# Performance work log

Hardware: AMD Instinct MI355X
Metric: run time of the kernel (lower is better)

The kernel has to match this reference:

```python
import jax, jax.numpy as jnp
import numpy as np

K_RATIO = 0.01
SIM_THRESHOLD = 0.6


def _gcn_update(feats, W_gcn, b_gcn):
    # feats: [N, C]. Build edges: inverse_similarity < (1 - thr)/2  <=>  cos sim > thr.
    nf = feats / jnp.maximum(jnp.linalg.norm(feats, axis=1, keepdims=True), 1e-12)
    sim = nf @ nf.T                                  # [N, N]
    inv_sim = (1.0 - sim) * 0.5
    adj = (inv_sim < (1.0 - SIM_THRESHOLD) * 0.5).astype(feats.dtype)  # includes self loops
    deg = jnp.sum(adj, axis=1)
    dinv = jax.lax.rsqrt(jnp.maximum(deg, 1.0))      # D^{-1/2}
    agg = dinv[:, None] * (adj @ (dinv[:, None] * feats))
    return agg @ W_gcn + b_gcn                        # [N, C]


def setup_inputs() -> dict:
    key = jax.random.key(0)
    k1, k2, k3 = jax.random.split(key, 3)
    B, C, H, W = 16, 128, 160, 160
    z = jax.random.normal(k1, (B, C, H, W), dtype=jnp.float32)
    score = jax.random.uniform(k2, (B, H, W), dtype=jnp.float32)
    W_gcn = jax.random.normal(k3, (C, C), dtype=jnp.float32) * (1.0 / np.sqrt(C))
    b_gcn = jnp.zeros((C,), dtype=jnp.float32)
    return {"z": z, "score": score, "W_gcn": W_gcn, "b_gcn": b_gcn}


def reference(z, score, W_gcn, b_gcn):
    B, C, H, W = z.shape
    num_select = int(H * W * K_RATIO)                # 256, static
    flat_score = score.reshape(B, H * W)
    _, top_idx = jax.lax.top_k(flat_score, num_select)   # [B, S]

    flat_z = z.reshape(B, C, H * W)
    idx_bcs = jnp.broadcast_to(top_idx[:, None, :], (B, C, num_select))
    top_features = jnp.take_along_axis(flat_z, idx_bcs, axis=2)  # [B, C, S]
    feats = top_features.transpose(0, 2, 1).reshape(B * num_select, C)  # [N, C]

    updated = _gcn_update(feats, W_gcn, b_gcn)        # [N, C]
    updated = updated.reshape(B, num_select, C).transpose(0, 2, 1)  # [B, C, S]

    b_ix = jnp.arange(B)[:, None, None]
    c_ix = jnp.arange(C)[None, :, None]
    new_flat = flat_z.at[b_ix, c_ix, top_idx[:, None, :]].set(updated)
    return new_flat.reshape(B, C, H, W)
```

## Files before the change

kernel.cpp:

```cpp
#include <hip/hip_runtime.h>
#include <hip/hip_bf16.h>

#define HWs 25600
#define NB 16
#define NC 128
#define NS 256
#define NN 4096
#define N4 13107200

#define K1_CPB 2880
#define K2_CPB 2240
#define K3_CPB 1280
#define CP_U 8
#define K2_BASE 5898240
#define K3_BASE 10485760

typedef __attribute__((ext_vector_type(8))) short bf16x8;
typedef __attribute__((ext_vector_type(4))) float f32x4;
typedef __attribute__((ext_vector_type(4))) int i32x4;
typedef unsigned long long u64;

template <int U>
__device__ __forceinline__ void copy_slice(const float4* __restrict__ zz,
                                           float4* __restrict__ oo,
                                           size_t base, int cb, int tid) {
  size_t start = base + (size_t)cb * (U * 256) + tid;
  float4 v[U];
  #pragma unroll
  for (int k = 0; k < U; ++k) v[k] = zz[start + k * 256];
  __builtin_amdgcn_sched_barrier(0);
  #pragma unroll
  for (int k = 0; k < U; ++k) oo[start + k * 256] = v[k];
}

__global__ __launch_bounds__(256) void k1_kernel(const float* __restrict__ z,
                                                 const float* __restrict__ score,
                                                 float* __restrict__ out,
                                                 int* __restrict__ sel) {
  __shared__ int hist[256];
  __shared__ int scan_s[256];
  __shared__ int scan_eq[256];
  __shared__ int bc_dig, bc_k;
  const int tid = threadIdx.x;
  const int bid = blockIdx.x;

  if (bid >= NB) {
    copy_slice<CP_U>((const float4*)z, (float4*)out, 0, bid - NB, tid);
    return;
  }

  int b = bid;
  const float* sc = score + (size_t)b * HWs;
  const float4* sc4 = (const float4*)sc;

  unsigned prefix = 0; int k = NS;
  for (int d = 3; d >= 0; --d) {
    int sh = d * 8;
    hist[tid] = 0; __syncthreads();
    unsigned maskHigh = (d == 3) ? 0u : (0xFFFFFFFFu << (sh + 8));
    #pragma unroll 5
    for (int i4 = 0; i4 < 25; ++i4) {
      float4 f = sc4[tid * 25 + i4];
      const float* fp = (const float*)&f;
      #pragma unroll
      for (int c = 0; c < 4; ++c) {
        unsigned v = __float_as_uint(fp[c]);
        if ((v & maskHigh) == prefix) atomicAdd(&hist[(v >> sh) & 255], 1);
      }
    }
    __syncthreads();
    int val = hist[255 - tid];
    scan_s[tid] = val; __syncthreads();
    for (int off = 1; off < 256; off <<= 1) {
      int a = (tid >= off) ? scan_s[tid - off] : 0;
      __syncthreads();
      scan_s[tid] += a; __syncthreads();
    }
    int q = 255 - tid;
    int Sq = scan_s[tid];
    int before = Sq - hist[q];
    if (before < k && k <= Sq) { bc_dig = q; bc_k = k - before; }
    __syncthreads();
    prefix |= ((unsigned)bc_dig) << sh;
    k = bc_k;
    __syncthreads();
  }
  unsigned t = prefix;

  int cgt = 0, ceq = 0;
  #pragma unroll 5
  for (int i4 = 0; i4 < 25; ++i4) {
    float4 f = sc4[tid * 25 + i4];
    const float* fp = (const float*)&f;
    #pragma unroll
    for (int c = 0; c < 4; ++c) {
      unsigned v = __float_as_uint(fp[c]);
      cgt += (v > t) ? 1 : 0;
      ceq += (v == t) ? 1 : 0;
    }
  }
  scan_s[tid] = cgt; scan_eq[tid] = ceq; __syncthreads();
  for (int off = 1; off < 256; off <<= 1) {
    int ag = (tid >= off) ? scan_s[tid - off] : 0;
    int ae = (tid >= off) ? scan_eq[tid - off] : 0;
    __syncthreads();
    scan_s[tid] += ag; scan_eq[tid] += ae; __syncthreads();
  }
  int total_gt = scan_s[255];
  int need = NS - total_gt;
  int g = scan_s[tid] - cgt;
  int e = scan_eq[tid] - ceq;
  for (int i4 = 0; i4 < 25; ++i4) {
    float4 f = sc4[tid * 25 + i4];
    const float* fp = (const float*)&f;
    #pragma unroll
    for (int c = 0; c < 4; ++c) {
      int i = tid * 100 + i4 * 4 + c;
      unsigned v = __float_as_uint(fp[c]);
      if (v > t) { sel[b * NS + g] = i; ++g; }
      else if (v == t) { if (e < need) sel[b * NS + total_gt + e] = i; ++e; }
    }
  }
}

__global__ __launch_bounds__(256) void k2_kernel(const float* __restrict__ z,
                                                 const int* __restrict__ sel,
                                                 float* __restrict__ out,
                                                 float* __restrict__ feats,
                                                 ushort* __restrict__ nfb) {
  const int tid = threadIdx.x;
  const int bid = blockIdx.x;
  if (bid >= NN / 4) {
    copy_slice<CP_U>((const float4*)z, (float4*)out, K2_BASE, bid - NN / 4, tid);
    return;
  }
  int row = bid * 4 + (tid >> 6);
  int lane = tid & 63;
  int b = row >> 8;
  int idx = sel[row];
  const float* zb = z + (size_t)b * NC * HWs + idx;
  float v0 = zb[(size_t)lane * HWs];
  float v1 = zb[(size_t)(lane + 64) * HWs];
  float ss = v0 * v0 + v1 * v1;
  #pragma unroll
  for (int off = 32; off; off >>= 1) ss += __shfl_xor(ss, off);
  float denom = fmaxf(sqrtf(ss), 1e-12f);
  feats[row * NC + lane] = v0;
  feats[row * NC + lane + 64] = v1;
  __hip_bfloat16 h0 = __float2bfloat16(v0 / denom);
  __hip_bfloat16 h1 = __float2bfloat16(v1 / denom);
  nfb[row * NC + lane] = *reinterpret_cast<ushort*>(&h0);
  nfb[row * NC + lane + 64] = *reinterpret_cast<ushort*>(&h1);
}

__global__ __launch_bounds__(256) void k3_kernel(const ushort* __restrict__ nfb,
                                                 const float* __restrict__ z,
                                                 float* __restrict__ out,
                                                 u64* __restrict__ adj) {
  __shared__ __align__(16) ushort tA[64 * 128];
  __shared__ __align__(16) ushort tB[64 * 128];
  __shared__ u64 rowbits[64];
  const int tid = threadIdx.x;
  const int bid = blockIdx.x;
  if (bid >= 4096) {
    copy_slice<CP_U>((const float4*)z, (float4*)out, K3_BASE, bid - 4096, tid);
    return;
  }
  int I0 = (bid & 63) * 64, J0 = (bid >> 6) * 64;
  if (tid < 64) rowbits[tid] = 0ull;
  for (int f = tid; f < 1024; f += 256) {
    int r = f >> 4, c = f & 15;
    int scnk = c ^ (r & 7);
    *(i32x4*)&tA[r * 128 + scnk * 8] = *(const i32x4*)(nfb + (size_t)(I0 + r) * NC + c * 8);
    *(i32x4*)&tB[r * 128 + scnk * 8] = *(const i32x4*)(nfb + (size_t)(J0 + r) * NC + c * 8);
  }
  __syncthreads();
  int w = tid >> 6, l = tid & 63;
  int r = l & 15, kg = l >> 4;
  f32x4 acc[4] = {{0.f, 0.f, 0.f, 0.f}, {0.f, 0.f, 0.f, 0.f},
                  {0.f, 0.f, 0.f, 0.f}, {0.f, 0.f, 0.f, 0.f}};
  int Ar = 16 * w + r;
  #pragma unroll
  for (int kk = 0; kk < 4; ++kk) {
    int chunkA = (kk * 4 + kg) ^ (Ar & 7);
    bf16x8 a = *(bf16x8*)&tA[Ar * 128 + chunkA * 8];
    #pragma unroll
    for (int j = 0; j < 4; ++j) {
      int Bc = 16 * j + r;
      int chunkB = (kk * 4 + kg) ^ (Bc & 7);
      bf16x8 bf = *(bf16x8*)&tB[Bc * 128 + chunkB * 8];
      acc[j] = __builtin_amdgcn_mfma_f32_16x16x32_bf16(a, bf, acc[j], 0, 0, 0);
    }
  }
  #pragma unroll
  for (int q = 0; q < 4; ++q) {
    u64 m = 0ull;
    #pragma unroll
    for (int j = 0; j < 4; ++j) {
      float simv = acc[j][q];
      if ((1.0f - simv) * 0.5f < 0.2f) m |= 1ull << (16 * j + (l & 15));
    }
    if (m) atomicOr(&rowbits[16 * w + (l >> 4) * 4 + q], m);
  }
  __syncthreads();
  if (tid < 64) adj[(size_t)(I0 + tid) * 64 + (bid >> 6)] = rowbits[tid];
}

__global__ __launch_bounds__(256) void k4_kernel(const u64* __restrict__ adj,
                                                 const float* __restrict__ feats,
                                                 const float* __restrict__ Wg,
                                                 const float* __restrict__ bg,
                                                 const int* __restrict__ sel,
                                                 float* __restrict__ out) {
  __shared__ __align__(16) float Wt[NC * 132];
  __shared__ __align__(16) float aggT[16 * 132];
  int tid = threadIdx.x;
  int r0 = blockIdx.x * 16;
  for (int f = tid; f < NC * NC; f += 256) {
    int c = f >> 7, cp = f & 127;
    Wt[cp * 132 + c] = Wg[f];
  }
  int w = tid >> 6, lane = tid & 63;
  for (int rr = 0; rr < 4; ++rr) {
    int lrow = w * 4 + rr;
    int row = r0 + lrow;
    u64 mw = adj[(size_t)row * 64 + lane];
    int ctot = __popcll(mw);
    #pragma unroll
    for (int off = 32; off; off >>= 1) ctot += __shfl_xor(ctot, off);
    float dinv_i = 1.0f / sqrtf(fmaxf((float)ctot, 1.0f));
    float acc0 = 0.f, acc1 = 0.f;
    for (int wi = 0; wi < 64; ++wi) {
      u64 w64 = __shfl((long long)mw, wi);
      while (w64) {
        int bit = __builtin_ctzll(w64);
        w64 &= w64 - 1;
        int j = wi * 64 + bit;
        u64 jm = adj[(size_t)j * 64 + lane];
        int cj = __popcll(jm);
        #pragma unroll
        for (int off = 32; off; off >>= 1) cj += __shfl_xor(cj, off);
        float dj = 1.0f / sqrtf(fmaxf((float)cj, 1.0f));
        acc0 += dj * feats[(size_t)j * NC + lane];
        acc1 += dj * feats[(size_t)j * NC + lane + 64];
      }
    }
    aggT[lrow * 132 + lane] = dinv_i * acc0;
    aggT[lrow * 132 + lane + 64] = dinv_i * acc1;
  }
  __syncthreads();
  int cp = tid & 127;
  int rsub = tid >> 7;
  float acc[8];
  float bb = bg[cp];
  #pragma unroll
  for (int q = 0; q < 8; ++q) acc[q] = bb;
  for (int c4 = 0; c4 < 32; ++c4) {
    float4 w4 = *(const float4*)&Wt[cp * 132 + c4 * 4];
    #pragma unroll
    for (int q = 0; q < 8; ++q) {
      float4 a4 = *(const float4*)&aggT[(rsub + 2 * q) * 132 + c4 * 4];
      acc[q] += a4.x * w4.x + a4.y * w4.y + a4.z * w4.z + a4.w * w4.w;
    }
  }
  #pragma unroll
  for (int q = 0; q < 8; ++q) {
    int row = r0 + rsub + 2 * q;
    int batch = row >> 8;
    int idx = sel[row];
    out[(size_t)(batch * NC + cp) * HWs + idx] = acc[q];
  }
}

extern "C" void kernel_launch(void* const* d_in, const int* in_sizes, int n_in,
                              void* d_out, int out_size, void* d_ws, size_t ws_size,
                              hipStream_t stream) {
  const float* z     = (const float*)d_in[0];
  const float* score = (const float*)d_in[1];
  const float* Wg    = (const float*)d_in[2];
  const float* bg    = (const float*)d_in[3];
  float* out = (float*)d_out;

  char* ws = (char*)d_ws;
  size_t off = 0;
  auto alloc = [&](size_t bytes) {
    void* p = ws + off;
    off = (off + bytes + 255) & ~(size_t)255;
    return p;
  };
  int* sel     = (int*)alloc(NN * sizeof(int));
  float* feats = (float*)alloc((size_t)NN * NC * sizeof(float));
  ushort* nfb  = (ushort*)alloc((size_t)NN * NC * sizeof(ushort));
  u64* adj     = (u64*)alloc((size_t)NN * 64 * sizeof(u64));

  k1_kernel<<<NB + K1_CPB, 256, 0, stream>>>(z, score, out, sel);
  k2_kernel<<<NN / 4 + K2_CPB, 256, 0, stream>>>(z, sel, out, feats, nfb);
  k3_kernel<<<4096 + K3_CPB, 256, 0, stream>>>(nfb, z, out, adj);
  k4_kernel<<<256, 256, 0, stream>>>(adj, feats, Wg, bg, sel, out);
}
```

Baseline: 178.1 us.

## Move full z copy into k1, use nontemporal stores, precompute degrees via atomics

```diff
diff --git a/kernel.cpp b/kernel.cpp
--- a/kernel.cpp
+++ b/kernel.cpp
@@ -7,13 +7,8 @@
 #define NS 256
 #define NN 4096
 #define N4 13107200
-
-#define K1_CPB 2880
-#define K2_CPB 2240
-#define K3_CPB 1280
 #define CP_U 8
-#define K2_BASE 5898240
-#define K3_BASE 10485760
+#define K1_CPB 6400
 
 typedef __attribute__((ext_vector_type(8))) short bf16x8;
 typedef __attribute__((ext_vector_type(4))) float f32x4;
@@ -23,14 +18,15 @@
 template <int U>
 __device__ __forceinline__ void copy_slice(const float4* __restrict__ zz,
                                            float4* __restrict__ oo,
-                                           size_t base, int cb, int tid) {
-  size_t start = base + (size_t)cb * (U * 256) + tid;
+                                           int cb, int tid) {
+  size_t start = (size_t)cb * (U * 256) + tid;
   float4 v[U];
   #pragma unroll
   for (int k = 0; k < U; ++k) v[k] = zz[start + k * 256];
   __builtin_amdgcn_sched_barrier(0);
   #pragma unroll
-  for (int k = 0; k < U; ++k) oo[start + k * 256] = v[k];
+  for (int k = 0; k < U; ++k)
+    __builtin_nontemporal_store(*(const f32x4*)&v[k], (f32x4*)&oo[start + k * 256]);
 }
 
 __global__ __launch_bounds__(256) void k1_kernel(const float* __restrict__ z,
@@ -45,7 +41,7 @@
   const int bid = blockIdx.x;
 
   if (bid >= NB) {
-    copy_slice<CP_U>((const float4*)z, (float4*)out, 0, bid - NB, tid);
+    copy_slice<CP_U>((const float4*)z, (float4*)out, bid - NB, tid);
     return;
   }
 
@@ -125,14 +121,13 @@
 
 __global__ __launch_bounds__(256) void k2_kernel(const float* __restrict__ z,
                                                  const int* __restrict__ sel,
-                                                 float* __restrict__ out,
                                                  float* __restrict__ feats,
-                                                 ushort* __restrict__ nfb) {
+                                                 ushort* __restrict__ nfb,
+                                                 int* __restrict__ deg) {
   const int tid = threadIdx.x;
   const int bid = blockIdx.x;
-  if (bid >= NN / 4) {
-    copy_slice<CP_U>((const float4*)z, (float4*)out, K2_BASE, bid - NN / 4, tid);
-    return;
+  if (bid < 4) {
+    *(i32x4*)&deg[bid * 1024 + tid * 4] = (i32x4){0, 0, 0, 0};
   }
   int row = bid * 4 + (tid >> 6);
   int lane = tid & 63;
@@ -154,18 +149,13 @@
 }
 
 __global__ __launch_bounds__(256) void k3_kernel(const ushort* __restrict__ nfb,
-                                                 const float* __restrict__ z,
-                                                 float* __restrict__ out,
-                                                 u64* __restrict__ adj) {
+                                                 u64* __restrict__ adj,
+                                                 int* __restrict__ deg) {
   __shared__ __align__(16) ushort tA[64 * 128];
   __shared__ __align__(16) ushort tB[64 * 128];
   __shared__ u64 rowbits[64];
   const int tid = threadIdx.x;
   const int bid = blockIdx.x;
-  if (bid >= 4096) {
-    copy_slice<CP_U>((const float4*)z, (float4*)out, K3_BASE, bid - 4096, tid);
-    return;
-  }
   int I0 = (bid & 63) * 64, J0 = (bid >> 6) * 64;
   if (tid < 64) rowbits[tid] = 0ull;
   for (int f = tid; f < 1024; f += 256) {
@@ -203,11 +193,16 @@
     if (m) atomicOr(&rowbits[16 * w + (l >> 4) * 4 + q], m);
   }
   __syncthreads();
-  if (tid < 64) adj[(size_t)(I0 + tid) * 64 + (bid >> 6)] = rowbits[tid];
+  if (tid < 64) {
+    u64 rb = rowbits[tid];
+    adj[(size_t)(I0 + tid) * 64 + (bid >> 6)] = rb;
+    atomicAdd(&deg[I0 + tid], __popcll(rb));
+  }
 }
 
 __global__ __launch_bounds__(256) void k4_kernel(const u64* __restrict__ adj,
                                                  const float* __restrict__ feats,
+                                                 const int* __restrict__ deg,
                                                  const float* __restrict__ Wg,
                                                  const float* __restrict__ bg,
                                                  const int* __restrict__ sel,
@@ -225,10 +220,7 @@
     int lrow = w * 4 + rr;
     int row = r0 + lrow;
     u64 mw = adj[(size_t)row * 64 + lane];
-    int ctot = __popcll(mw);
-    #pragma unroll
-    for (int off = 32; off; off >>= 1) ctot += __shfl_xor(ctot, off);
-    float dinv_i = 1.0f / sqrtf(fmaxf((float)ctot, 1.0f));
+    float dinv_i = 1.0f / sqrtf(fmaxf((float)deg[row], 1.0f));
     float acc0 = 0.f, acc1 = 0.f;
     for (int wi = 0; wi < 64; ++wi) {
       u64 w64 = __shfl((long long)mw, wi);
@@ -236,11 +228,7 @@
         int bit = __builtin_ctzll(w64);
         w64 &= w64 - 1;
         int j = wi * 64 + bit;
-        u64 jm = adj[(size_t)j * 64 + lane];
-        int cj = __popcll(jm);
-        #pragma unroll
-        for (int off = 32; off; off >>= 1) cj += __shfl_xor(cj, off);
-        float dj = 1.0f / sqrtf(fmaxf((float)cj, 1.0f));
+        float dj = 1.0f / sqrtf(fmaxf((float)deg[j], 1.0f));
         acc0 += dj * feats[(size_t)j * NC + lane];
         acc1 += dj * feats[(size_t)j * NC + lane + 64];
       }
@@ -292,9 +280,10 @@
   float* feats = (float*)alloc((size_t)NN * NC * sizeof(float));
   ushort* nfb  = (ushort*)alloc((size_t)NN * NC * sizeof(ushort));
   u64* adj     = (u64*)alloc((size_t)NN * 64 * sizeof(u64));
+  int* deg     = (int*)alloc(NN * sizeof(int));
 
   k1_kernel<<<NB + K1_CPB, 256, 0, stream>>>(z, score, out, sel);
-  k2_kernel<<<NN / 4 + K2_CPB, 256, 0, stream>>>(z, sel, out, feats, nfb);
-  k3_kernel<<<4096 + K3_CPB, 256, 0, stream>>>(nfb, z, out, adj);
-  k4_kernel<<<256, 256, 0, stream>>>(adj, feats, Wg, bg, sel, out);
-}
+  k2_kernel<<<NN / 4, 256, 0, stream>>>(z, sel, feats, nfb, deg);
+  k3_kernel<<<4096, 256, 0, stream>>>(nfb, adj, deg);
+  k4_kernel<<<256, 256, 0, stream>>>(adj, feats, deg, Wg, bg, sel, out);
+}
```

Measured after the change: 164.0 us. -7.9%, faster.
